# Optimization experiments

Measured on AMD Instinct MI355X. Metric: run time of the kernel, lower is better.

Reference implementation:

```python
import jax, jax.numpy as jnp
import numpy as np

STRIDE = (1, 1)
PADDING = ((1, 1), (1, 1))


def setup_inputs() -> dict:
    key = jax.random.key(0)
    kx, kw, kb = jax.random.split(key, 3)
    x = jax.random.normal(kx, (32, 128, 56, 56), dtype=jnp.float32)
    weight = jax.random.normal(kw, (256, 128, 3, 3), dtype=jnp.float32)  # (O, I, kh, kw)
    bias = jax.random.normal(kb, (256,), dtype=jnp.float32)
    return {"x": x, "weight": weight, "bias": bias}


def reference(x, weight, bias):
    # Faithful dense 2D convolution (cross-correlation, as in the torch module),
    # NCHW input, OIHW weight, stride 1, padding 1.
    out = jax.lax.conv_general_dilated(
        x, weight,
        window_strides=STRIDE,
        padding=PADDING,
        dimension_numbers=("NCHW", "OIHW", "NCHW"),
    )
    return out + bias[None, :, None, None]
```

## Files before the change

### kernel.cpp

```cpp
#include <hip/hip_runtime.h>

#define C_IN   128
#define H_IN   56
#define W_IN   56
#define HW     3136
#define CHW    401408
#define O_OUT  256
#define OHW    802816

#define LDK 72

typedef __bf16 bf16x8 __attribute__((ext_vector_type(8)));
typedef float  f32x4  __attribute__((ext_vector_type(4)));
typedef unsigned short ushort_t;
typedef ushort_t ushort8 __attribute__((ext_vector_type(8)));

__device__ __forceinline__ ushort_t f2bf(float f) {
    union { float f; unsigned u; } v; v.f = f;
    unsigned r = (v.u + 0x7fffu + ((v.u >> 16) & 1u)) >> 16;
    return (ushort_t)r;
}

__global__ void wt3_kernel(const float* __restrict__ w, ushort_t* __restrict__ wbf) {
    int idx = blockIdx.x * 256 + threadIdx.x;
    if (idx >= 9 * 256 * 128) return;
    int pos = idx >> 15;
    int rem = idx & 32767;
    int o   = rem >> 7;
    int c   = rem & 127;
    int s   = pos * 2 + (c >> 6);
    wbf[((s * 256 + o) << 6) + (c & 63)] = f2bf(w[o * 1152 + c * 9 + pos]);
}

__global__ __launch_bounds__(256, 2)
void conv6_kernel(const float* __restrict__ x, const ushort_t* __restrict__ wbf,
                  const float* __restrict__ bias, float* __restrict__ out) {
    __shared__ ushort_t patch[232 * 128];

    const int tid  = threadIdx.x;
    const int lane = tid & 63;
    const int wave = tid >> 6;
    const int l15  = lane & 15;
    const int quad = lane >> 4;
    const int om   = wave * 64;

    int b = blockIdx.x;
    b = (b & 7) * 112 + (b >> 3);
    const int n  = b / 28;
    const int h0 = (b - n * 28) * 2;

    if (tid < 232) {
        const int pr = tid / 58;
        const int wp = tid - pr * 58;
        const int ih = h0 - 1 + pr;
        const int iw = wp - 1;
        const bool ok = ((unsigned)ih < 56u) && ((unsigned)iw < 56u);
        const float* xs = x + (size_t)n * CHW + ih * W_IN + iw;
        ushort_t* dst = patch + tid * 128;
        const int wkey = wp & 7;
        #pragma unroll
        for (int cg = 0; cg < 16; ++cg) {
            ushort8 v;
            #pragma unroll
            for (int j = 0; j < 8; ++j) {
                float f = 0.0f;
                if (ok) f = xs[(size_t)(cg * 8 + j) * HW];
                v[j] = f2bf(f);
            }
            *(ushort8*)(dst + (((cg ^ wkey)) << 3)) = v;
        }
    }
    __syncthreads();

    int ppix[7], wk[7], obo[7];
    #pragma unroll
    for (int u = 0; u < 7; ++u) {
        int pix = u * 16 + l15;
        int pr  = (pix >= 56) ? 1 : 0;
        int ww  = pix - pr * 56;
        ppix[u] = (pr * 58 + ww) * 128;
        wk[u]   = ww;
        obo[u]  = (h0 + pr) * W_IN + ww;
    }

    int aoff[4];
    #pragma unroll
    for (int t = 0; t < 4; ++t)
        aoff[t] = ((om + t * 16 + l15) << 6) + (quad << 3);

    f32x4 acc[4][7];
    #pragma unroll
    for (int t = 0; t < 4; ++t)
        #pragma unroll
        for (int u = 0; u < 7; ++u)
            acc[t][u] = f32x4{0.f, 0.f, 0.f, 0.f};

    for (int kh = 0; kh < 3; ++kh) {
        #pragma unroll
        for (int kw = 0; kw < 3; ++kw) {
            const int poff = (kh * 58 + kw) * 128;
            #pragma unroll
            for (int half = 0; half < 2; ++half) {
                const int s = (kh * 3 + kw) * 2 + half;
                const ushort_t* wsp = wbf + (size_t)s * 16384;
                #pragma unroll
                for (int ks = 0; ks < 2; ++ks) {
                    bf16x8 af[4], bfv[7];
                    #pragma unroll
                    for (int t = 0; t < 4; ++t)
                        af[t] = *(const bf16x8*)(wsp + aoff[t] + ks * 32);
                    const int k16 = half * 8 + ks * 4 + quad;
                    #pragma unroll
                    for (int u = 0; u < 7; ++u) {
                        const int slot = k16 ^ ((wk[u] + kw) & 7);
                        bfv[u] = *(const bf16x8*)(patch + ppix[u] + poff + (slot << 3));
                    }
                    #pragma unroll
                    for (int t = 0; t < 4; ++t)
                        #pragma unroll
                        for (int u = 0; u < 7; ++u)
                            acc[t][u] = __builtin_amdgcn_mfma_f32_16x16x32_bf16(
                                            af[t], bfv[u], acc[t][u], 0, 0, 0);
                }
            }
        }
    }

    f32x4 bv[4];
    #pragma unroll
    for (int t = 0; t < 4; ++t)
        bv[t] = *(const f32x4*)(bias + om + t * 16 + quad * 4);
    float* outn = out + (size_t)n * OHW;
    #pragma unroll
    for (int u = 0; u < 7; ++u) {
        float* op = outn + obo[u];
        #pragma unroll
        for (int t = 0; t < 4; ++t) {
            const int o0 = om + t * 16 + quad * 4;
            #pragma unroll
            for (int r = 0; r < 4; ++r)
                op[(size_t)(o0 + r) * HW] = acc[t][u][r] + bv[t][r];
        }
    }
}


__global__ void wt_kernel(const float* __restrict__ w, ushort_t* __restrict__ wbf) {
    int idx = blockIdx.x * 256 + threadIdx.x;
    if (idx >= 9 * 256 * 128) return;
    int pos = idx >> 15;
    int rem = idx & 32767;
    int o   = rem >> 7;
    int c   = rem & 127;
    wbf[idx] = f2bf(w[o * 1152 + c * 9 + pos]);
}

__global__ __launch_bounds__(512, 4)
void conv_kernel(const float* __restrict__ x, const ushort_t* __restrict__ wbf,
                 const float* __restrict__ bias, float* __restrict__ out) {
    __shared__ ushort_t As[256 * LDK];
    __shared__ ushort_t Bs[128 * LDK];

    const int tid  = threadIdx.x;
    const int lane = tid & 63;
    const int wave = tid >> 6;
    const int wm   = wave >> 1;
    const int wn   = wave & 1;
    const int l15  = lane & 15;
    const int quad = lane >> 4;

    const int pix_base = blockIdx.x * 128;
    const int px  = tid & 127;
    const int cg0 = tid >> 7;
    const int p   = pix_base + px;
    const int n_img = p / HW;
    const int hw    = p - n_img * HW;
    const int h     = hw / W_IN;
    const int w_    = hw - h * W_IN;
    const float* ximg = x + (long)n_img * CHW;

    f32x4 acc[4][4];
    #pragma unroll
    for (int t = 0; t < 4; ++t)
        #pragma unroll
        for (int u = 0; u < 4; ++u)
            acc[t][u] = f32x4{0.f, 0.f, 0.f, 0.f};

    for (int pos = 0; pos < 9; ++pos) {
        const int dh = pos / 3 - 1;
        const int dw = pos - (pos / 3) * 3 - 1;
        const int ih = h + dh;
        const int iw = w_ + dw;
        const bool valid = ((unsigned)ih < (unsigned)H_IN) && ((unsigned)iw < (unsigned)W_IN);
        const float* xsrc = ximg + ih * W_IN + iw;

        for (int half = 0; half < 2; ++half) {
            const int c0 = half * 64;
            {
                const ushort_t* wsrc = wbf + ((pos * 256) << 7) + c0;
                #pragma unroll
                for (int sj = 0; sj < 4; ++sj) {
                    const int o  = (tid >> 3) + sj * 64;
                    const int cg = tid & 7;
                    ushort8 v = *(const ushort8*)(wsrc + (o << 7) + cg * 8);
                    *(ushort8*)(&As[o * LDK + cg * 8]) = v;
                }
            }
            {
                #pragma unroll
                for (int sj = 0; sj < 2; ++sj) {
                    const int cg = cg0 + sj * 4;
                    const float* src = xsrc + (long)(c0 + cg * 8) * HW;
                    ushort8 v;
                    #pragma unroll
                    for (int j = 0; j < 8; ++j) {
                        float f = valid ? src[j * HW] : 0.0f;
                        v[j] = f2bf(f);
                    }
                    *(ushort8*)(&Bs[px * LDK + cg * 8]) = v;
                }
            }
            __syncthreads();

            #pragma unroll
            for (int ks = 0; ks < 2; ++ks) {
                bf16x8 af[4], bfv[4];
                #pragma unroll
                for (int t = 0; t < 4; ++t) {
                    const int row = wm * 64 + t * 16 + l15;
                    af[t] = *(const bf16x8*)(&As[row * LDK + ks * 32 + quad * 8]);
                }
                #pragma unroll
                for (int u = 0; u < 4; ++u) {
                    const int col = wn * 64 + u * 16 + l15;
                    bfv[u] = *(const bf16x8*)(&Bs[col * LDK + ks * 32 + quad * 8]);
                }
                #pragma unroll
                for (int t = 0; t < 4; ++t)
                    #pragma unroll
                    for (int u = 0; u < 4; ++u)
                        acc[t][u] = __builtin_amdgcn_mfma_f32_16x16x32_bf16(af[t], bfv[u], acc[t][u], 0, 0, 0);
            }
            __syncthreads();
        }
    }

    #pragma unroll
    for (int u = 0; u < 4; ++u) {
        const int col = wn * 64 + u * 16 + l15;
        const int pp  = pix_base + col;
        const int hw2 = pp - (pp / HW) * HW;
        const long obase = (long)(pp / HW) * OHW + hw2;
        #pragma unroll
        for (int t = 0; t < 4; ++t) {
            const int o_base = wm * 64 + t * 16 + quad * 4;
            #pragma unroll
            for (int r = 0; r < 4; ++r) {
                const int o = o_base + r;
                out[obase + (long)o * HW] = acc[t][u][r] + bias[o];
            }
        }
    }
}

extern "C" void kernel_launch(void* const* d_in, const int* in_sizes, int n_in,
                              void* d_out, int out_size, void* d_ws, size_t ws_size,
                              hipStream_t stream) {
    const float* x    = (const float*)d_in[0];
    const float* w    = (const float*)d_in[1];
    const float* bias = (const float*)d_in[2];
    float* out        = (float*)d_out;

    ushort_t* wbf = (ushort_t*)d_ws;

    if (ws_size >= 589824u) {
        hipLaunchKernelGGL(wt3_kernel, dim3(1152), dim3(256), 0, stream, w, wbf);
        hipLaunchKernelGGL(conv6_kernel, dim3(896), dim3(256), 0, stream,
                           x, wbf, bias, out);
    } else {
        hipLaunchKernelGGL(wt_kernel, dim3(1152), dim3(256), 0, stream, w, wbf);
        hipLaunchKernelGGL(conv_kernel, dim3(100352 / 128), dim3(512), 0, stream,
                           x, wbf, bias, out);
    }
}
```

Baseline: 226.9 us.

## Stage weights through LDS triple-buffered ring with async global-to-LDS loads, larger tiles

Each block now covers four output rows with 512 threads (eight waves split two ways over output channels and two ways over pixels), so the input patch is shared across more output pixels. Weights are re-laid out and streamed into a three-slot LDS ring via global_load_lds, prefetching two K-steps ahead with explicit vmcnt waits and barriers. MFMA issue is wrapped in raised wave priority. This aims to replace per-wave global weight loads with shared LDS reads and to overlap weight fetching with compute. In exchange the grid halves to 448 blocks, LDS use grows, and every K-step adds a block-wide barrier.

```diff
diff --git a/kernel.cpp b/kernel.cpp
--- a/kernel.cpp
+++ b/kernel.cpp
@@ -21,35 +21,47 @@
     return (ushort_t)r;
 }
 
-__global__ void wt3_kernel(const float* __restrict__ w, ushort_t* __restrict__ wbf) {
+typedef const __attribute__((address_space(1))) unsigned int* gas_ptr;
+typedef __attribute__((address_space(3))) unsigned int* las_ptr;
+__device__ __forceinline__ void gl_lds16(const void* g, void* l) {
+    __builtin_amdgcn_global_load_lds((gas_ptr)g, (las_ptr)l, 16, 0, 0);
+}
+
+__global__ void wt4_kernel(const float* __restrict__ w, ushort_t* __restrict__ wbf) {
     int idx = blockIdx.x * 256 + threadIdx.x;
-    if (idx >= 9 * 256 * 128) return;
-    int pos = idx >> 15;
-    int rem = idx & 32767;
-    int o   = rem >> 7;
-    int c   = rem & 127;
-    int s   = pos * 2 + (c >> 6);
-    wbf[((s * 256 + o) << 6) + (c & 63)] = f2bf(w[o * 1152 + c * 9 + pos]);
-}
-
-__global__ __launch_bounds__(256, 2)
-void conv6_kernel(const float* __restrict__ x, const ushort_t* __restrict__ wbf,
-                  const float* __restrict__ bias, float* __restrict__ out) {
-    __shared__ ushort_t patch[232 * 128];
+    if (idx >= 294912) return;
+    int q  = idx >> 13;
+    int r  = idx & 8191;
+    int k8 = r >> 11;
+    int o  = (r >> 3) & 255;
+    int e  = r & 7;
+    int c  = (q & 3) * 32 + k8 * 8 + e;
+    int pos = q >> 2;
+    wbf[idx] = f2bf(w[o * 1152 + c * 9 + pos]);
+}
+
+__global__ __launch_bounds__(512, 2)
+void conv10_kernel(const float* __restrict__ x, const ushort_t* __restrict__ wbf,
+                   const float* __restrict__ bias, float* __restrict__ out) {
+    __shared__ ushort_t patch[348 * 128];
+    __shared__ ushort_t ring[3][8192];
 
     const int tid  = threadIdx.x;
     const int lane = tid & 63;
     const int wave = tid >> 6;
+    const int wm   = wave >> 1;
+    const int wn   = wave & 1;
     const int l15  = lane & 15;
     const int quad = lane >> 4;
-    const int om   = wave * 64;
+    const int om   = wm * 64;
+    const int wbase = wave << 10;
 
     int b = blockIdx.x;
-    b = (b & 7) * 112 + (b >> 3);
-    const int n  = b / 28;
-    const int h0 = (b - n * 28) * 2;
-
-    if (tid < 232) {
+    b = (b & 7) * 56 + (b >> 3);
+    const int n  = b / 14;
+    const int h0 = (b - n * 14) * 4;
+
+    if (tid < 348) {
         const int pr = tid / 58;
         const int wp = tid - pr * 58;
         const int ih = h0 - 1 + pr;
@@ -67,27 +79,32 @@
                 if (ok) f = xs[(size_t)(cg * 8 + j) * HW];
                 v[j] = f2bf(f);
             }
-            *(ushort8*)(dst + (((cg ^ wkey)) << 3)) = v;
-        }
-    }
+            *(ushort8*)(dst + ((cg ^ wkey) << 3)) = v;
+        }
+    }
+    {
+        const char* wg = (const char*)wbf;
+        #pragma unroll
+        for (int qq = 0; qq < 2; ++qq)
+            #pragma unroll
+            for (int j = 0; j < 2; ++j)
+                gl_lds16(wg + qq * 16384 + j * 8192 + wbase + (lane << 4),
+                         (char*)ring[qq] + j * 8192 + wbase);
+    }
+    asm volatile("s_waitcnt vmcnt(0)" ::: "memory");
     __syncthreads();
 
     int ppix[7], wk[7], obo[7];
     #pragma unroll
     for (int u = 0; u < 7; ++u) {
-        int pix = u * 16 + l15;
-        int pr  = (pix >= 56) ? 1 : 0;
+        int pix = wn * 112 + u * 16 + l15;
+        int pr  = pix / 56;
         int ww  = pix - pr * 56;
         ppix[u] = (pr * 58 + ww) * 128;
         wk[u]   = ww;
         obo[u]  = (h0 + pr) * W_IN + ww;
     }
 
-    int aoff[4];
-    #pragma unroll
-    for (int t = 0; t < 4; ++t)
-        aoff[t] = ((om + t * 16 + l15) << 6) + (quad << 3);
-
     f32x4 acc[4][7];
     #pragma unroll
     for (int t = 0; t < 4; ++t)
@@ -95,35 +112,50 @@
         for (int u = 0; u < 7; ++u)
             acc[t][u] = f32x4{0.f, 0.f, 0.f, 0.f};
 
-    for (int kh = 0; kh < 3; ++kh) {
-        #pragma unroll
-        for (int kw = 0; kw < 3; ++kw) {
-            const int poff = (kh * 58 + kw) * 128;
-            #pragma unroll
-            for (int half = 0; half < 2; ++half) {
-                const int s = (kh * 3 + kw) * 2 + half;
-                const ushort_t* wsp = wbf + (size_t)s * 16384;
-                #pragma unroll
-                for (int ks = 0; ks < 2; ++ks) {
-                    bf16x8 af[4], bfv[7];
-                    #pragma unroll
-                    for (int t = 0; t < 4; ++t)
-                        af[t] = *(const bf16x8*)(wsp + aoff[t] + ks * 32);
-                    const int k16 = half * 8 + ks * 4 + quad;
-                    #pragma unroll
-                    for (int u = 0; u < 7; ++u) {
-                        const int slot = k16 ^ ((wk[u] + kw) & 7);
-                        bfv[u] = *(const bf16x8*)(patch + ppix[u] + poff + (slot << 3));
-                    }
-                    #pragma unroll
-                    for (int t = 0; t < 4; ++t)
-                        #pragma unroll
-                        for (int u = 0; u < 7; ++u)
-                            acc[t][u] = __builtin_amdgcn_mfma_f32_16x16x32_bf16(
-                                            af[t], bfv[u], acc[t][u], 0, 0, 0);
-                }
-            }
-        }
+    ushort_t* r0 = ring[0];
+    ushort_t* r1 = ring[1];
+    ushort_t* r2 = ring[2];
+
+    for (int q = 0; q < 36; ++q) {
+        if (q < 34) {
+            const char* src = (const char*)wbf + (size_t)(q + 2) * 16384;
+            char* d = (char*)r2;
+            gl_lds16(src + wbase + (lane << 4),        d + wbase);
+            gl_lds16(src + 8192 + wbase + (lane << 4), d + 8192 + wbase);
+        }
+
+        const int pos = q >> 2;
+        const int kh  = pos / 3;
+        const int kw  = pos - kh * 3;
+        const int poff = (kh * 58 + kw) * 128;
+        const int cg   = (q & 3) * 4 + quad;
+
+        bf16x8 af[4], bfv[7];
+        #pragma unroll
+        for (int t = 0; t < 4; ++t)
+            af[t] = *(const bf16x8*)(r0 + quad * 2048 + (om + t * 16 + l15) * 8);
+        #pragma unroll
+        for (int u = 0; u < 7; ++u) {
+            const int slot = cg ^ ((wk[u] + kw) & 7);
+            bfv[u] = *(const bf16x8*)(patch + ppix[u] + poff + (slot << 3));
+        }
+
+        __builtin_amdgcn_s_setprio(1);
+        #pragma unroll
+        for (int t = 0; t < 4; ++t)
+            #pragma unroll
+            for (int u = 0; u < 7; ++u)
+                acc[t][u] = __builtin_amdgcn_mfma_f32_16x16x32_bf16(
+                                af[t], bfv[u], acc[t][u], 0, 0, 0);
+        __builtin_amdgcn_s_setprio(0);
+
+        __builtin_amdgcn_sched_barrier(0);
+        if (q < 34) asm volatile("s_waitcnt vmcnt(2)" ::: "memory");
+        else        asm volatile("s_waitcnt vmcnt(0)" ::: "memory");
+        __builtin_amdgcn_s_barrier();
+        __builtin_amdgcn_sched_barrier(0);
+
+        ushort_t* tmp = r0; r0 = r1; r1 = r2; r2 = tmp;
     }
 
     f32x4 bv[4];
@@ -274,8 +306,8 @@
     ushort_t* wbf = (ushort_t*)d_ws;
 
     if (ws_size >= 589824u) {
-        hipLaunchKernelGGL(wt3_kernel, dim3(1152), dim3(256), 0, stream, w, wbf);
-        hipLaunchKernelGGL(conv6_kernel, dim3(896), dim3(256), 0, stream,
+        hipLaunchKernelGGL(wt4_kernel, dim3(1152), dim3(256), 0, stream, w, wbf);
+        hipLaunchKernelGGL(conv10_kernel, dim3(448), dim3(512), 0, stream,
                            x, wbf, bias, out);
     } else {
         hipLaunchKernelGGL(wt_kernel, dim3(1152), dim3(256), 0, stream, w, wbf);
```

Result: faster. 214.8 us (-5.3%).

## Pre-transpose input to padded NHWC bf16 and stream tiles via global_load_lds

Applied to the files above, without the earlier changes.

Adds a separate kernel that converts the NCHW fp32 input into a zero-padded, channel-swizzled NHWC bf16 buffer in workspace. The conv kernel becomes a 128x128 implicit-GEMM tile that loads weight and input slices straight into LDS with global_load_lds across 18 K-steps. Swizzling is also applied to the weight layout. This removes the strided per-channel scalar gathers and in-kernel conversion, but costs an extra full pass over the input, a large workspace requirement and extra sync per K-step.

```diff
diff --git a/kernel.cpp b/kernel.cpp
--- a/kernel.cpp
+++ b/kernel.cpp
@@ -9,6 +9,7 @@
 #define OHW    802816
 
 #define LDK 72
+#define XTP 132
 
 typedef __bf16 bf16x8 __attribute__((ext_vector_type(8)));
 typedef float  f32x4  __attribute__((ext_vector_type(4)));
@@ -21,125 +22,191 @@
     return (ushort_t)r;
 }
 
-__global__ void wt3_kernel(const float* __restrict__ w, ushort_t* __restrict__ wbf) {
+typedef const __attribute__((address_space(1))) unsigned int* gas_ptr;
+typedef __attribute__((address_space(3))) unsigned int* las_ptr;
+__device__ __forceinline__ void gl_lds16(const void* g, void* l) {
+    __builtin_amdgcn_global_load_lds((gas_ptr)g, (las_ptr)l, 16, 0, 0);
+}
+
+
+__global__ void wt2_kernel(const float* __restrict__ w, ushort_t* __restrict__ wbf) {
     int idx = blockIdx.x * 256 + threadIdx.x;
     if (idx >= 9 * 256 * 128) return;
     int pos = idx >> 15;
     int rem = idx & 32767;
     int o   = rem >> 7;
     int c   = rem & 127;
-    int s   = pos * 2 + (c >> 6);
-    wbf[((s * 256 + o) << 6) + (c & 63)] = f2bf(w[o * 1152 + c * 9 + pos]);
-}
-
-__global__ __launch_bounds__(256, 2)
-void conv6_kernel(const float* __restrict__ x, const ushort_t* __restrict__ wbf,
-                  const float* __restrict__ bias, float* __restrict__ out) {
-    __shared__ ushort_t patch[232 * 128];
+    int s    = pos * 2 + (c >> 6);
+    int slot = ((c >> 3) & 7) ^ (o & 7);
+    wbf[((s * 256 + o) << 6) + (slot << 3) + (c & 7)] = f2bf(w[o * 1152 + c * 9 + pos]);
+}
+
+__global__ __launch_bounds__(256)
+void xt2_kernel(const float* __restrict__ x, ushort_t* __restrict__ xbp) {
+    const int b  = blockIdx.x;
+    const int n  = b / 58;
+    const int hp = b - n * 58;
+    ushort_t* orow = xbp + (size_t)(n * 58 + hp) * 7424;
+    const int t = threadIdx.x;
+    ushort8 z = ushort8{0,0,0,0,0,0,0,0};
+
+    if (hp == 0 || hp == 57) {
+        #pragma unroll
+        for (int i = 0; i < 4; ++i) {
+            int u = i * 256 + t;
+            if (u < 928) *(ushort8*)(orow + u * 8) = z;
+        }
+        return;
+    }
+
+    __shared__ ushort_t T[56 * XTP];
+    const int h = hp - 1;
+    const float* src = x + (size_t)n * CHW + h * W_IN;
+    #pragma unroll
+    for (int i = 0; i < 7; ++i) {
+        int g  = i * 256 + t;
+        int c  = g / 14;
+        int f4 = g - c * 14;
+        f32x4 v = *(const f32x4*)(src + (size_t)c * HW + f4 * 4);
+        #pragma unroll
+        for (int j = 0; j < 4; ++j)
+            T[(f4 * 4 + j) * XTP + c] = f2bf(v[j]);
+    }
+    __syncthreads();
+    #pragma unroll
+    for (int i = 0; i < 4; ++i) {
+        int u = i * 256 + t;
+        if (u < 928) {
+            int wp = u >> 4, gg = u & 15;
+            ushort8 v = (wp == 0 || wp == 57) ? z
+                        : *(const ushort8*)(&T[(wp - 1) * XTP + gg * 8]);
+            *(ushort8*)(orow + wp * 128 + ((gg ^ (wp & 7)) << 3)) = v;
+        }
+    }
+}
+
+__global__ __launch_bounds__(256, 3)
+void conv12_kernel(const ushort_t* __restrict__ xbp, const ushort_t* __restrict__ wbf,
+                   const float* __restrict__ bias, float* __restrict__ out) {
+    __shared__ ushort_t As[128 * 64];
+    __shared__ ushort_t Bs[128 * 64];
 
     const int tid  = threadIdx.x;
     const int lane = tid & 63;
     const int wave = tid >> 6;
+    const int wm   = wave >> 1;
+    const int wn   = wave & 1;
     const int l15  = lane & 15;
     const int quad = lane >> 4;
-    const int om   = wave * 64;
-
-    int b = blockIdx.x;
-    b = (b & 7) * 112 + (b >> 3);
-    const int n  = b / 28;
-    const int h0 = (b - n * 28) * 2;
-
-    if (tid < 232) {
-        const int pr = tid / 58;
-        const int wp = tid - pr * 58;
-        const int ih = h0 - 1 + pr;
-        const int iw = wp - 1;
-        const bool ok = ((unsigned)ih < 56u) && ((unsigned)iw < 56u);
-        const float* xs = x + (size_t)n * CHW + ih * W_IN + iw;
-        ushort_t* dst = patch + tid * 128;
-        const int wkey = wp & 7;
-        #pragma unroll
-        for (int cg = 0; cg < 16; ++cg) {
-            ushort8 v;
-            #pragma unroll
-            for (int j = 0; j < 8; ++j) {
-                float f = 0.0f;
-                if (ok) f = xs[(size_t)(cg * 8 + j) * HW];
-                v[j] = f2bf(f);
-            }
-            *(ushort8*)(dst + (((cg ^ wkey)) << 3)) = v;
-        }
-    }
-    __syncthreads();
-
-    int ppix[7], wk[7], obo[7];
-    #pragma unroll
-    for (int u = 0; u < 7; ++u) {
-        int pix = u * 16 + l15;
-        int pr  = (pix >= 56) ? 1 : 0;
-        int ww  = pix - pr * 56;
-        ppix[u] = (pr * 58 + ww) * 128;
-        wk[u]   = ww;
-        obo[u]  = (h0 + pr) * W_IN + ww;
+    const int om   = wm * 64;
+
+    int tau = blockIdx.x;
+    tau = (tau & 7) * 196 + (tau >> 3);
+    const int pix_base = (tau >> 1) * 128;
+    const int ob       = (tau & 1) << 7;
+
+    long Bc[4];
+    {
+        #pragma unroll
+        for (int c = 0; c < 4; ++c) {
+            int idx = (wave * 4 + c) * 64 + lane;
+            int px  = idx >> 3;
+            int j8  = idx & 7;
+            int p   = pix_base + px;
+            int n_  = p / HW;
+            int hw  = p - n_ * HW;
+            int h   = hw / W_IN;
+            int w_  = hw - h * W_IN;
+            Bc[c] = (long)(n_ * 58 + h + 1) * 14848 + (long)(w_ + 1) * 256 + j8 * 16;
+        }
     }
 
     int aoff[4];
     #pragma unroll
+    for (int t = 0; t < 4; ++t) {
+        int ol = om + t * 16 + l15;
+        aoff[t] = ol * 128 + ((quad ^ (ol & 7)) << 4);
+    }
+    int pxb[4], pr7[4], obo[4];
+    #pragma unroll
+    for (int u = 0; u < 4; ++u) {
+        int pxr = wn * 64 + u * 16 + l15;
+        int p   = pix_base + pxr;
+        pxb[u]  = pxr * 128;
+        pr7[u]  = (p + 1) & 7;
+        obo[u]  = p;
+    }
+
+    f32x4 acc[4][4];
+    #pragma unroll
     for (int t = 0; t < 4; ++t)
-        aoff[t] = ((om + t * 16 + l15) << 6) + (quad << 3);
-
-    f32x4 acc[4][7];
-    #pragma unroll
-    for (int t = 0; t < 4; ++t)
-        #pragma unroll
-        for (int u = 0; u < 7; ++u)
+        #pragma unroll
+        for (int u = 0; u < 4; ++u)
             acc[t][u] = f32x4{0.f, 0.f, 0.f, 0.f};
 
-    for (int kh = 0; kh < 3; ++kh) {
-        #pragma unroll
-        for (int kw = 0; kw < 3; ++kw) {
-            const int poff = (kh * 58 + kw) * 128;
-            #pragma unroll
-            for (int half = 0; half < 2; ++half) {
-                const int s = (kh * 3 + kw) * 2 + half;
-                const ushort_t* wsp = wbf + (size_t)s * 16384;
-                #pragma unroll
-                for (int ks = 0; ks < 2; ++ks) {
-                    bf16x8 af[4], bfv[7];
-                    #pragma unroll
-                    for (int t = 0; t < 4; ++t)
-                        af[t] = *(const bf16x8*)(wsp + aoff[t] + ks * 32);
-                    const int k16 = half * 8 + ks * 4 + quad;
-                    #pragma unroll
-                    for (int u = 0; u < 7; ++u) {
-                        const int slot = k16 ^ ((wk[u] + kw) & 7);
-                        bfv[u] = *(const bf16x8*)(patch + ppix[u] + poff + (slot << 3));
-                    }
-                    #pragma unroll
-                    for (int t = 0; t < 4; ++t)
-                        #pragma unroll
-                        for (int u = 0; u < 7; ++u)
-                            acc[t][u] = __builtin_amdgcn_mfma_f32_16x16x32_bf16(
-                                            af[t], bfv[u], acc[t][u], 0, 0, 0);
-                }
-            }
-        }
-    }
-
-    f32x4 bv[4];
-    #pragma unroll
-    for (int t = 0; t < 4; ++t)
-        bv[t] = *(const f32x4*)(bias + om + t * 16 + quad * 4);
-    float* outn = out + (size_t)n * OHW;
-    #pragma unroll
-    for (int u = 0; u < 7; ++u) {
-        float* op = outn + obo[u];
+    const char* xg = (const char*)xbp;
+    const char* wg = (const char*)wbf;
+    char* AsB = (char*)As;
+    char* BsB = (char*)Bs;
+
+    for (int q = 0; q < 18; ++q) {
+        const int pos  = q >> 1;
+        const int half = q & 1;
+        const int dh   = pos / 3 - 1;
+        const int dw   = pos - (pos / 3) * 3 - 1;
+        const long soff = (long)dh * 14848 + (long)dw * 256 + half * 128;
+
+        {
+            const char* as = wg + (size_t)q * 32768 + (size_t)ob * 128;
+            #pragma unroll
+            for (int j = 0; j < 4; ++j) {
+                const int blk = (wave * 4 + j) * 1024;
+                gl_lds16(as + blk + (lane << 4), AsB + blk);
+                gl_lds16(xg + Bc[j] + soff,      BsB + blk);
+            }
+        }
+        __syncthreads();
+
+        int boff[4];
+        #pragma unroll
+        for (int u = 0; u < 4; ++u) {
+            const int key = (pr7[u] + dw + 8) & 7;
+            boff[u] = pxb[u] + ((quad ^ key) << 4);
+        }
+        #pragma unroll
+        for (int ks = 0; ks < 2; ++ks) {
+            const int kx = ks << 6;
+            bf16x8 af[4], bf[4];
+            #pragma unroll
+            for (int t = 0; t < 4; ++t)
+                af[t] = *(const bf16x8*)(AsB + (aoff[t] ^ kx));
+            #pragma unroll
+            for (int u = 0; u < 4; ++u)
+                bf[u] = *(const bf16x8*)(BsB + (boff[u] ^ kx));
+            #pragma unroll
+            for (int t = 0; t < 4; ++t)
+                #pragma unroll
+                for (int u = 0; u < 4; ++u)
+                    acc[t][u] = __builtin_amdgcn_mfma_f32_16x16x32_bf16(
+                                    af[t], bf[u], acc[t][u], 0, 0, 0);
+        }
+        __syncthreads();
+    }
+
+    #pragma unroll
+    for (int u = 0; u < 4; ++u) {
+        const int pp  = obo[u];
+        const int nn  = pp / HW;
+        const int hw2 = pp - nn * HW;
+        const long obase = (long)nn * OHW + hw2;
         #pragma unroll
         for (int t = 0; t < 4; ++t) {
-            const int o0 = om + t * 16 + quad * 4;
-            #pragma unroll
-            for (int r = 0; r < 4; ++r)
-                op[(size_t)(o0 + r) * HW] = acc[t][u][r] + bv[t][r];
+            const int o_base = ob + wm * 64 + t * 16 + quad * 4;
+            #pragma unroll
+            for (int r = 0; r < 4; ++r) {
+                const int o = o_base + r;
+                out[obase + (long)o * HW] = acc[t][u][r] + bias[o];
+            }
         }
     }
 }
@@ -271,13 +338,17 @@
     const float* bias = (const float*)d_in[2];
     float* out        = (float*)d_out;
 
-    ushort_t* wbf = (ushort_t*)d_ws;
-
-    if (ws_size >= 589824u) {
-        hipLaunchKernelGGL(wt3_kernel, dim3(1152), dim3(256), 0, stream, w, wbf);
-        hipLaunchKernelGGL(conv6_kernel, dim3(896), dim3(256), 0, stream,
-                           x, wbf, bias, out);
+    const size_t NEED_NEW = 589824u + 27557888u;
+
+    if (ws_size >= NEED_NEW) {
+        ushort_t* wbf = (ushort_t*)d_ws;
+        ushort_t* xbp = (ushort_t*)((char*)d_ws + 589824);
+        hipLaunchKernelGGL(wt2_kernel, dim3(1152), dim3(256), 0, stream, w, wbf);
+        hipLaunchKernelGGL(xt2_kernel, dim3(1856), dim3(256), 0, stream, x, xbp);
+        hipLaunchKernelGGL(conv12_kernel, dim3(1568), dim3(256), 0, stream,
+                           xbp, wbf, bias, out);
     } else {
+        ushort_t* wbf = (ushort_t*)d_ws;
         hipLaunchKernelGGL(wt_kernel, dim3(1152), dim3(256), 0, stream, w, wbf);
         hipLaunchKernelGGL(conv_kernel, dim3(100352 / 128), dim3(512), 0, stream,
                            x, wbf, bias, out);
```

New measurement: 209.6 us. 1.08x faster.
